# Kernel optimization log

Measured on AMD Instinct MI355X. Metric: run time of the kernel, lower is better.

## Reference

```python
import jax, jax.numpy as jnp
import numpy as np

N = 8192
IN_F = 512
OUT_F = 64
NEG_SLOPE = 0.01  # nn.LeakyReLU default
MASK_VAL = -1e9


def setup_inputs() -> dict:
    key = jax.random.key(0)
    k_h, k_adj, k_W, k_a = jax.random.split(key, 4)
    h = jax.random.normal(k_h, (N, IN_F), dtype=jnp.float32)
    adjacency = jax.random.randint(k_adj, (N, N), 0, 2, dtype=jnp.int32)
    # xavier_uniform bounds
    bW = float(np.sqrt(6.0 / (IN_F + OUT_F)))
    ba = float(np.sqrt(6.0 / (2 * OUT_F + 1)))
    W = jax.random.uniform(k_W, (IN_F, OUT_F), minval=-bW, maxval=bW, dtype=jnp.float32)
    a = jax.random.uniform(k_a, (2 * OUT_F, 1), minval=-ba, maxval=ba, dtype=jnp.float32)
    return {"h": h, "adjacency": adjacency, "W": W, "a": a}


def reference(h, adjacency, W, a):
    WH = h @ W                                  # [N, out_f]
    wh1 = WH @ a[:OUT_F, :]                     # [N, 1]
    wh2 = WH @ a[OUT_F:, :]                     # [N, 1]
    e = jax.nn.leaky_relu(wh1 + wh2.T, negative_slope=NEG_SLOPE)  # [N, N]
    attnt = jnp.where(adjacency > 0, e, jnp.float32(MASK_VAL))
    attnt = jax.nn.softmax(attnt, axis=1)       # row-wise softmax
    hfirst = attnt @ WH                         # [N, out_f]
    return jax.nn.elu(hfirst)
```

## Files before the change

kernel.cpp:

```cpp
#include <hip/hip_runtime.h>
#include <hip/hip_bf16.h>

#define N 8192
#define IN_F 512
#define OUT_F 64
#define S_SPLIT 16
#define JT (N / S_SPLIT)
#define LOG2E 1.4426950408889634f

typedef __attribute__((ext_vector_type(8))) short short8;
typedef __attribute__((ext_vector_type(4))) float floatx4;
typedef __attribute__((ext_vector_type(4))) int intx4;
typedef unsigned long long ull;

__device__ inline short f2bf(float x) {
    __hip_bfloat16 b = __float2bfloat16(x);
    return __builtin_bit_cast(short, b);
}

__global__ __launch_bounds__(256) void k_pack(const int* __restrict__ adj,
                                              unsigned* __restrict__ mask) {
    int wv = (blockIdx.x * 256 + threadIdx.x) >> 6;
    int lane = threadIdx.x & 63;
    const int* p = adj + (size_t)wv * 512 + lane;
    ull m0 = __ballot(p[0]   > 0);
    ull m1 = __ballot(p[64]  > 0);
    ull m2 = __ballot(p[128] > 0);
    ull m3 = __ballot(p[192] > 0);
    ull m4 = __ballot(p[256] > 0);
    ull m5 = __ballot(p[320] > 0);
    ull m6 = __ballot(p[384] > 0);
    ull m7 = __ballot(p[448] > 0);
    if (lane < 16) {
        ull s0 = (lane & 2) ? m1 : m0;
        ull s1 = (lane & 2) ? m3 : m2;
        ull s2 = (lane & 2) ? m5 : m4;
        ull s3 = (lane & 2) ? m7 : m6;
        ull t0 = (lane & 4) ? s1 : s0;
        ull t1 = (lane & 4) ? s3 : s2;
        ull u  = (lane & 8) ? t1 : t0;
        unsigned dw = (lane & 1) ? (unsigned)(u >> 32) : (unsigned)u;
        mask[wv * 16 + lane] = dw;
    }
}

__global__ void k_wt(const float* __restrict__ W, short* __restrict__ WT) {
    int idx = blockIdx.x * 256 + threadIdx.x;
    int k = idx >> 6, f = idx & 63;
    WT[f * IN_F + k] = f2bf(W[k * OUT_F + f]);
}

__global__ __launch_bounds__(64) void k_wh(const float* __restrict__ h,
                                           const short* __restrict__ WT,
                                           const float* __restrict__ a,
                                           short* __restrict__ WHbT,
                                           float* __restrict__ wh1s,
                                           float* __restrict__ wh2s) {
    __shared__ float tile[OUT_F][17];
    int lane = threadIdx.x;
    int n = lane & 15, q = lane >> 4;
    int i0 = blockIdx.x * 16;
    int rowA = i0 + n;
    const float* hp = h + (size_t)rowA * IN_F + q * 8;
    floatx4 acc[4] = {};
    for (int k0 = 0; k0 < IN_F; k0 += 32) {
        floatx4 h0 = *(const floatx4*)(hp + k0);
        floatx4 h1 = *(const floatx4*)(hp + k0 + 4);
        short8 af;
#pragma unroll
        for (int j = 0; j < 4; j++) { af[j] = f2bf(h0[j]); af[j + 4] = f2bf(h1[j]); }
#pragma unroll
        for (int b = 0; b < 4; b++) {
            short8 bf_ = *(const short8*)(WT + (b * 16 + n) * IN_F + k0 + q * 8);
            acc[b] = __builtin_amdgcn_mfma_f32_16x16x32_bf16(af, bf_, acc[b], 0, 0, 0);
        }
    }
#pragma unroll
    for (int b = 0; b < 4; b++)
#pragma unroll
        for (int r = 0; r < 4; r++)
            tile[b * 16 + n][q * 4 + r] = acc[b][r];
    float a1v[4], a2v[4];
#pragma unroll
    for (int b = 0; b < 4; b++) { a1v[b] = a[b * 16 + n]; a2v[b] = a[OUT_F + b * 16 + n]; }
#pragma unroll
    for (int r = 0; r < 4; r++) {
        float s1 = 0.f, s2 = 0.f;
#pragma unroll
        for (int b = 0; b < 4; b++) { s1 += acc[b][r] * a1v[b]; s2 += acc[b][r] * a2v[b]; }
#pragma unroll
        for (int m = 1; m <= 8; m <<= 1) {
            s1 += __shfl_xor(s1, m, 64);
            s2 += __shfl_xor(s2, m, 64);
        }
        if (n == 0) {
            wh1s[i0 + q * 4 + r] = s1 * LOG2E;
            wh2s[i0 + q * 4 + r] = s2 * LOG2E;
        }
    }
    __syncthreads();
    const float* tc = tile[lane];
    short8 s0, s1v;
#pragma unroll
    for (int k = 0; k < 8; k++) { s0[k] = f2bf(tc[k]); s1v[k] = f2bf(tc[k + 8]); }
    *(short8*)(WHbT + (size_t)lane * N + i0) = s0;
    *(short8*)(WHbT + (size_t)lane * N + i0 + 8) = s1v;
}

__global__ __launch_bounds__(256) void k_bp(const short* __restrict__ WHbT,
                                            short* __restrict__ BP) {
    int g = blockIdx.x;
    int b = threadIdx.x >> 6;
    int lane = threadIdx.x & 63;
    int n = lane & 15, q = lane >> 4;
    short8 v = *(const short8*)(WHbT + (size_t)(b * 16 + n) * N + g * 32 + q * 8);
    *(short8*)(BP + ((size_t)(g * 4 + b) * 64 + lane) * 8) = v;
}

__global__ __launch_bounds__(256) void k_attn(const unsigned* __restrict__ maskb,
                                              const short* __restrict__ BP,
                                              const float* __restrict__ wh1s,
                                              const float* __restrict__ wh2s,
                                              float* __restrict__ num_part,
                                              float* __restrict__ den_part) {
    int tid = threadIdx.x;
    int w = tid >> 6;
    int lane = tid & 63;
    int n = lane & 15, q = lane >> 4, qs = q * 8;
    int split = blockIdx.y;
    int j0 = split * JT;
    int i0 = blockIdx.x * 256 + w * 64;

    float wh1f[4];
#pragma unroll
    for (int rf = 0; rf < 4; rf++) wh1f[rf] = wh1s[i0 + rf * 16 + n];

    floatx4 acc[4][4] = {};
    floatx4 accd[4] = {};
    const float* w2p = wh2s + j0 + qs;
    const short8* bp = (const short8*)BP + (size_t)split * 4096 + lane;
    short8 ones;
#pragma unroll
    for (int k = 0; k < 8; k++) ones[k] = (short)0x3F80;

    intx4 mcur[4], mnxt[4];
#pragma unroll
    for (int rf = 0; rf < 4; rf++)
        mcur[rf] = *(const intx4*)(maskb + (size_t)(i0 + rf * 16 + n) * 256 + split * 16);

    for (int g = 0; g < 4; g++) {
        if (g < 3) {
#pragma unroll
            for (int rf = 0; rf < 4; rf++)
                mnxt[rf] = *(const intx4*)(maskb + (size_t)(i0 + rf * 16 + n) * 256
                                           + split * 16 + (g + 1) * 4);
        }
#pragma unroll
        for (int d = 0; d < 4; d++) {
            int s = g * 4 + d;
            short8 bfr[4];
#pragma unroll
            for (int b = 0; b < 4; b++)
                bfr[b] = bp[s * 256 + b * 64];
            floatx4 w20 = *(const floatx4*)(w2p + s * 32);
            floatx4 w21 = *(const floatx4*)(w2p + s * 32 + 4);
#pragma unroll
            for (int rf = 0; rf < 4; rf++) {
                unsigned md = (unsigned)mcur[rf][d];
                short8 af;
#pragma unroll
                for (int jj = 0; jj < 8; jj++) {
                    float x = wh1f[rf] + ((jj < 4) ? w20[jj] : w21[jj - 4]);
                    float t = fmaxf(x, 0.01f * x);
                    float e = __builtin_amdgcn_exp2f(t);
                    af[jj] = f2bf(((md >> (qs + jj)) & 1u) ? e : 0.f);
                }
#pragma unroll
                for (int b = 0; b < 4; b++)
                    acc[rf][b] = __builtin_amdgcn_mfma_f32_16x16x32_bf16(af, bfr[b], acc[rf][b], 0, 0, 0);
                accd[rf] = __builtin_amdgcn_mfma_f32_16x16x32_bf16(af, ones, accd[rf], 0, 0, 0);
            }
        }
#pragma unroll
        for (int rf = 0; rf < 4; rf++) mcur[rf] = mnxt[rf];
    }

#pragma unroll
    for (int rf = 0; rf < 4; rf++) {
        if (n == 0) {
#pragma unroll
            for (int r = 0; r < 4; r++)
                den_part[(size_t)split * N + i0 + rf * 16 + q * 4 + r] = accd[rf][r];
        }
    }
    float* np_ = num_part + (size_t)split * N * OUT_F;
#pragma unroll
    for (int rf = 0; rf < 4; rf++)
#pragma unroll
        for (int b = 0; b < 4; b++)
#pragma unroll
            for (int r = 0; r < 4; r++)
                np_[(size_t)(i0 + rf * 16 + q * 4 + r) * OUT_F + b * 16 + n] = acc[rf][b][r];
}

__global__ void k_final(const float* __restrict__ num_part,
                        const float* __restrict__ den_part,
                        float* __restrict__ out) {
    int idx = blockIdx.x * 256 + threadIdx.x;
    int row = idx >> 6;
    float s = 0.f, d = 0.f;
#pragma unroll
    for (int sp = 0; sp < S_SPLIT; sp++) {
        s += num_part[(size_t)sp * N * OUT_F + idx];
        d += den_part[sp * N + row];
    }
    float x = s / d;
    out[idx] = (x > 0.f) ? x : (__expf(x) - 1.f);
}

extern "C" void kernel_launch(void* const* d_in, const int* in_sizes, int n_in,
                              void* d_out, int out_size, void* d_ws, size_t ws_size,
                              hipStream_t stream) {
    const float* h = (const float*)d_in[0];
    const int* adj = (const int*)d_in[1];
    const float* W = (const float*)d_in[2];
    const float* a = (const float*)d_in[3];
    float* out = (float*)d_out;

    char* ws = (char*)d_ws;
    short* WHbT     = (short*)(ws);
    short* WT       = (short*)(ws + (size_t)(1 << 20));
    float* wh1s     = (float*)(ws + (size_t)(1 << 20) + (64 << 10));
    float* wh2s     = wh1s + N;
    unsigned* maskb = (unsigned*)(ws + (size_t)(2 << 20));
    short* BP       = (short*)(ws + (size_t)(12 << 20));
    float* num_p    = (float*)(ws + (size_t)(16 << 20));
    float* den_p    = (float*)(ws + (size_t)(48 << 20));

    k_pack<<<dim3((N / 32) * (N / 256) * 4), dim3(256), 0, stream>>>(adj, maskb);
    k_wt<<<dim3(128), dim3(256), 0, stream>>>(W, WT);
    k_wh<<<dim3(N / 16), dim3(64), 0, stream>>>(h, WT, a, WHbT, wh1s, wh2s);
    k_bp<<<dim3(256), dim3(256), 0, stream>>>(WHbT, BP);
    k_attn<<<dim3(N / 256, S_SPLIT), dim3(256), 0, stream>>>(maskb, BP, wh1s, wh2s,
                                                             num_p, den_p);
    k_final<<<dim3((N * OUT_F) / 256), dim3(256), 0, stream>>>(num_p, den_p, out);
}
```

Before: 412.8 us.

## Factor exp of leaky-relu into per-node exponentials and shrink attention tiles

The exponential of the leaky-relu score is rewritten as max(exp(a_i)exp(b_j), exp(0.01a_i)exp(0.01b_j)), so k_wh precomputes four per-node exponential vectors and k_attn uses multiplies and a max instead of a transcendental per element. k_attn now gives each wave 16 rows instead of 64, which quadruples the grid, and adds a launch-bounds occupancy hint plus software prefetch of the next B fragment and column factors. Bf16 conversion uses a manual round-half-up perm trick rather than the library conversion. Risks: the products can overflow or underflow where the direct exp would not, and each B fragment is now reused by fewer rows.

```diff
diff --git a/kernel.cpp b/kernel.cpp
--- a/kernel.cpp
+++ b/kernel.cpp
@@ -54,8 +54,10 @@
                                            const short* __restrict__ WT,
                                            const float* __restrict__ a,
                                            short* __restrict__ WHbT,
-                                           float* __restrict__ wh1s,
-                                           float* __restrict__ wh2s) {
+                                           float* __restrict__ P1,
+                                           float* __restrict__ p1,
+                                           float* __restrict__ P2,
+                                           float* __restrict__ p2) {
     __shared__ float tile[OUT_F][17];
     int lane = threadIdx.x;
     int n = lane & 15, q = lane >> 4;
@@ -94,8 +96,11 @@
             s2 += __shfl_xor(s2, m, 64);
         }
         if (n == 0) {
-            wh1s[i0 + q * 4 + r] = s1 * LOG2E;
-            wh2s[i0 + q * 4 + r] = s2 * LOG2E;
+            int i = i0 + q * 4 + r;
+            P1[i] = __builtin_amdgcn_exp2f(LOG2E * s1);
+            p1[i] = __builtin_amdgcn_exp2f(0.01f * LOG2E * s1);
+            P2[i] = __builtin_amdgcn_exp2f(LOG2E * s2);
+            p2[i] = __builtin_amdgcn_exp2f(0.01f * LOG2E * s2);
         }
     }
     __syncthreads();
@@ -117,90 +122,91 @@
     *(short8*)(BP + ((size_t)(g * 4 + b) * 64 + lane) * 8) = v;
 }
 
-__global__ __launch_bounds__(256) void k_attn(const unsigned* __restrict__ maskb,
-                                              const short* __restrict__ BP,
-                                              const float* __restrict__ wh1s,
-                                              const float* __restrict__ wh2s,
-                                              float* __restrict__ num_part,
-                                              float* __restrict__ den_part) {
+__global__ __launch_bounds__(256, 4) void k_attn(const unsigned* __restrict__ maskb,
+                                                 const short* __restrict__ BP,
+                                                 const float* __restrict__ P1,
+                                                 const float* __restrict__ p1,
+                                                 const float* __restrict__ P2,
+                                                 const float* __restrict__ p2,
+                                                 float* __restrict__ num_part,
+                                                 float* __restrict__ den_part) {
     int tid = threadIdx.x;
     int w = tid >> 6;
     int lane = tid & 63;
     int n = lane & 15, q = lane >> 4, qs = q * 8;
     int split = blockIdx.y;
     int j0 = split * JT;
-    int i0 = blockIdx.x * 256 + w * 64;
-
-    float wh1f[4];
-#pragma unroll
-    for (int rf = 0; rf < 4; rf++) wh1f[rf] = wh1s[i0 + rf * 16 + n];
-
-    floatx4 acc[4][4] = {};
-    floatx4 accd[4] = {};
-    const float* w2p = wh2s + j0 + qs;
+    int i0 = blockIdx.x * 64 + w * 16;
+    int row = i0 + n;
+
+    float P1f = P1[row], p1f = p1[row];
+    const unsigned* mrow = maskb + (size_t)row * 256 + split * 16;
     const short8* bp = (const short8*)BP + (size_t)split * 4096 + lane;
+    const float* P2p = P2 + j0 + qs;
+    const float* p2p = p2 + j0 + qs;
+
+    floatx4 acc[4] = {};
+    floatx4 accd = {};
     short8 ones;
 #pragma unroll
     for (int k = 0; k < 8; k++) ones[k] = (short)0x3F80;
 
-    intx4 mcur[4], mnxt[4];
-#pragma unroll
-    for (int rf = 0; rf < 4; rf++)
-        mcur[rf] = *(const intx4*)(maskb + (size_t)(i0 + rf * 16 + n) * 256 + split * 16);
-
-    for (int g = 0; g < 4; g++) {
-        if (g < 3) {
-#pragma unroll
-            for (int rf = 0; rf < 4; rf++)
-                mnxt[rf] = *(const intx4*)(maskb + (size_t)(i0 + rf * 16 + n) * 256
-                                           + split * 16 + (g + 1) * 4);
-        }
-#pragma unroll
-        for (int d = 0; d < 4; d++) {
-            int s = g * 4 + d;
-            short8 bfr[4];
-#pragma unroll
-            for (int b = 0; b < 4; b++)
-                bfr[b] = bp[s * 256 + b * 64];
-            floatx4 w20 = *(const floatx4*)(w2p + s * 32);
-            floatx4 w21 = *(const floatx4*)(w2p + s * 32 + 4);
-#pragma unroll
-            for (int rf = 0; rf < 4; rf++) {
-                unsigned md = (unsigned)mcur[rf][d];
-                short8 af;
-#pragma unroll
-                for (int jj = 0; jj < 8; jj++) {
-                    float x = wh1f[rf] + ((jj < 4) ? w20[jj] : w21[jj - 4]);
-                    float t = fmaxf(x, 0.01f * x);
-                    float e = __builtin_amdgcn_exp2f(t);
-                    af[jj] = f2bf(((md >> (qs + jj)) & 1u) ? e : 0.f);
-                }
-#pragma unroll
-                for (int b = 0; b < 4; b++)
-                    acc[rf][b] = __builtin_amdgcn_mfma_f32_16x16x32_bf16(af, bfr[b], acc[rf][b], 0, 0, 0);
-                accd[rf] = __builtin_amdgcn_mfma_f32_16x16x32_bf16(af, ones, accd[rf], 0, 0, 0);
-            }
-        }
-#pragma unroll
-        for (int rf = 0; rf < 4; rf++) mcur[rf] = mnxt[rf];
-    }
-
-#pragma unroll
-    for (int rf = 0; rf < 4; rf++) {
-        if (n == 0) {
-#pragma unroll
-            for (int r = 0; r < 4; r++)
-                den_part[(size_t)split * N + i0 + rf * 16 + q * 4 + r] = accd[rf][r];
-        }
+    short8 bfr[4];
+#pragma unroll
+    for (int b = 0; b < 4; b++) bfr[b] = bp[b * 64];
+    floatx4 Pc0 = *(const floatx4*)(P2p);
+    floatx4 Pc1 = *(const floatx4*)(P2p + 4);
+    floatx4 pc0 = *(const floatx4*)(p2p);
+    floatx4 pc1 = *(const floatx4*)(p2p + 4);
+
+    for (int s = 0; s < 16; s++) {
+        int sn = (s + 1) & 15;
+        short8 nb[4];
+#pragma unroll
+        for (int b = 0; b < 4; b++) nb[b] = bp[sn * 256 + b * 64];
+        floatx4 nP0 = *(const floatx4*)(P2p + sn * 32);
+        floatx4 nP1 = *(const floatx4*)(P2p + sn * 32 + 4);
+        floatx4 np0 = *(const floatx4*)(p2p + sn * 32);
+        floatx4 np1 = *(const floatx4*)(p2p + sn * 32 + 4);
+
+        unsigned mds = mrow[s] >> qs;
+        float pv[8];
+#pragma unroll
+        for (int jj = 0; jj < 8; jj++) {
+            float hv = P1f * ((jj < 4) ? Pc0[jj] : Pc1[jj - 4]);
+            float lv = p1f * ((jj < 4) ? pc0[jj] : pc1[jj - 4]);
+            float mx = fmaxf(hv, lv);
+            pv[jj] = (mds & (1u << jj)) ? mx : 0.f;
+        }
+        intx4 ai;
+#pragma unroll
+        for (int k = 0; k < 4; k++) {
+            unsigned u0 = __builtin_bit_cast(unsigned, pv[2 * k]) + 0x8000u;
+            unsigned u1 = __builtin_bit_cast(unsigned, pv[2 * k + 1]) + 0x8000u;
+            ai[k] = (int)__builtin_amdgcn_perm(u1, u0, 0x07060302u);
+        }
+        short8 af = __builtin_bit_cast(short8, ai);
+#pragma unroll
+        for (int b = 0; b < 4; b++)
+            acc[b] = __builtin_amdgcn_mfma_f32_16x16x32_bf16(af, bfr[b], acc[b], 0, 0, 0);
+        accd = __builtin_amdgcn_mfma_f32_16x16x32_bf16(af, ones, accd, 0, 0, 0);
+
+#pragma unroll
+        for (int b = 0; b < 4; b++) bfr[b] = nb[b];
+        Pc0 = nP0; Pc1 = nP1; pc0 = np0; pc1 = np1;
+    }
+
+    if (n == 0) {
+#pragma unroll
+        for (int r = 0; r < 4; r++)
+            den_part[(size_t)split * N + i0 + q * 4 + r] = accd[r];
     }
     float* np_ = num_part + (size_t)split * N * OUT_F;
 #pragma unroll
-    for (int rf = 0; rf < 4; rf++)
-#pragma unroll
-        for (int b = 0; b < 4; b++)
-#pragma unroll
-            for (int r = 0; r < 4; r++)
-                np_[(size_t)(i0 + rf * 16 + q * 4 + r) * OUT_F + b * 16 + n] = acc[rf][b][r];
+    for (int b = 0; b < 4; b++)
+#pragma unroll
+        for (int r = 0; r < 4; r++)
+            np_[(size_t)(i0 + q * 4 + r) * OUT_F + b * 16 + n] = acc[b][r];
 }
 
 __global__ void k_final(const float* __restrict__ num_part,
@@ -230,8 +236,10 @@
     char* ws = (char*)d_ws;
     short* WHbT     = (short*)(ws);
     short* WT       = (short*)(ws + (size_t)(1 << 20));
-    float* wh1s     = (float*)(ws + (size_t)(1 << 20) + (64 << 10));
-    float* wh2s     = wh1s + N;
+    float* P1       = (float*)(ws + (size_t)(1 << 20) + (64 << 10));
+    float* p1       = P1 + N;
+    float* P2       = p1 + N;
+    float* p2       = P2 + N;
     unsigned* maskb = (unsigned*)(ws + (size_t)(2 << 20));
     short* BP       = (short*)(ws + (size_t)(12 << 20));
     float* num_p    = (float*)(ws + (size_t)(16 << 20));
@@ -239,9 +247,9 @@
 
     k_pack<<<dim3((N / 32) * (N / 256) * 4), dim3(256), 0, stream>>>(adj, maskb);
     k_wt<<<dim3(128), dim3(256), 0, stream>>>(W, WT);
-    k_wh<<<dim3(N / 16), dim3(64), 0, stream>>>(h, WT, a, WHbT, wh1s, wh2s);
+    k_wh<<<dim3(N / 16), dim3(64), 0, stream>>>(h, WT, a, WHbT, P1, p1, P2, p2);
     k_bp<<<dim3(256), dim3(256), 0, stream>>>(WHbT, BP);
-    k_attn<<<dim3(N / 256, S_SPLIT), dim3(256), 0, stream>>>(maskb, BP, wh1s, wh2s,
-                                                             num_p, den_p);
+    k_attn<<<dim3(N / 64, S_SPLIT), dim3(256), 0, stream>>>(maskb, BP, P1, p1, P2, p2,
+                                                            num_p, den_p);
     k_final<<<dim3((N * OUT_F) / 256), dim3(256), 0, stream>>>(num_p, den_p, out);
 }
```

Result: slower. 433.4 us (+5.0%).
